# Kernel tuning notes

Measured on AMD Instinct MI355X. Metric: run time of the kernel, lower is better.

Reference implementation:

```python
import jax, jax.numpy as jnp
import numpy as np

N_NODES = 100000
N_EDGES = 1600000
EDGE_FEAT = 16
EDGE_HID = 32
NODE_FEAT = 128


def setup_inputs() -> dict:
    key = jax.random.key(0)
    ks = jax.random.split(key, 10)
    inp = {
        "edge_logits": jax.random.normal(ks[0], (N_EDGES, 1), dtype=jnp.float32),
        "edge_feats": jax.random.normal(ks[1], (N_EDGES, EDGE_FEAT), dtype=jnp.float32),
        "node_feats": jax.random.normal(ks[2], (N_NODES, NODE_FEAT), dtype=jnp.float32),
        "dst": jax.random.randint(ks[3], (N_EDGES,), 0, N_NODES, dtype=jnp.int32),
        # edge_transform Linear(edge_feat -> edge_hid)
        "W_et": jax.random.normal(ks[4], (EDGE_FEAT, EDGE_HID), dtype=jnp.float32) * (1.0 / np.sqrt(EDGE_FEAT)),
        "b_et": jnp.zeros((EDGE_HID,), dtype=jnp.float32),
        # MLP Linear(edge_hid + node_feat -> node_feat)
        "W1": jax.random.normal(ks[5], (EDGE_HID + NODE_FEAT, NODE_FEAT), dtype=jnp.float32) * (1.0 / np.sqrt(EDGE_HID + NODE_FEAT)),
        "b1": jnp.zeros((NODE_FEAT,), dtype=jnp.float32),
        # MLP Linear(node_feat -> node_feat)
        "W2": jax.random.normal(ks[6], (NODE_FEAT, NODE_FEAT), dtype=jnp.float32) * (1.0 / np.sqrt(NODE_FEAT)),
        "b2": jnp.zeros((NODE_FEAT,), dtype=jnp.float32),
    }
    return inp


def reference(edge_logits, edge_feats, node_feats, dst, W_et, b_et, W1, b1, W2, b2):
    # edge_softmax: segment softmax of edge_logits grouped by destination node
    logits = edge_logits[:, 0]                                        # [E]
    seg_max = jax.ops.segment_max(logits, dst, num_segments=N_NODES)  # [N]
    seg_max = jnp.where(jnp.isfinite(seg_max), seg_max, 0.0)          # guard empty segments
    ex = jnp.exp(logits - seg_max[dst])                               # [E]
    denom = jax.ops.segment_sum(ex, dst, num_segments=N_NODES)        # [N]
    denom = jnp.where(denom == 0.0, 1.0, denom)
    alpha = ex / denom[dst]                                           # [E]
    # edge transform (dropout is identity in eval) then weight by attention
    e = alpha[:, None] * (edge_feats @ W_et + b_et)                   # [E, H]
    # scatter-sum aggregation to destination nodes
    c = jax.ops.segment_sum(e, dst, num_segments=N_NODES)             # [N, H]
    context = jax.nn.elu(c)
    h = jnp.concatenate([context, node_feats], axis=1)                # [N, H+F]
    h = jax.nn.relu(h @ W1 + b1)
    return jax.nn.relu(h @ W2 + b2)                                   # [N, F]
```

## Files before the change

### kernel.cpp

```cpp
#include <hip/hip_runtime.h>

#define EF 16
#define EH 32
#define NF 128
#define K1 160
#define HS 168
#define H2S 136

typedef __attribute__((ext_vector_type(8))) short bf16x8;
typedef __attribute__((ext_vector_type(4))) float f32x4;

__device__ __forceinline__ unsigned short f2b(float f) {
  unsigned u = __float_as_uint(f);
  u += 0x7FFFu + ((u >> 16) & 1u);
  return (unsigned short)(u >> 16);
}
__device__ __forceinline__ unsigned pack2b(float a, float b) {
  return (unsigned)f2b(a) | ((unsigned)f2b(b) << 16);
}

__global__ void k_init(unsigned* __restrict__ cnt, int n,
                       const float* __restrict__ W1, const float* __restrict__ W2,
                       unsigned short* __restrict__ w1t, unsigned short* __restrict__ w2t) {
  int i = blockIdx.x * blockDim.x + threadIdx.x;
  if (i < n) cnt[i] = 0u;
  if (i < K1 * NF) {
    int nn = i / K1, k = i % K1;
    w1t[i] = f2b(W1[k * NF + nn]);
  } else if (i < K1 * NF + NF * NF) {
    int j = i - K1 * NF;
    int nn = j / NF, k = j % NF;
    w2t[j] = f2b(W2[k * NF + nn]);
  }
}

__global__ void k_hist(const int* __restrict__ dst, unsigned* __restrict__ cnt,
                       unsigned* __restrict__ rank, int n_edges) {
  int e = blockIdx.x * blockDim.x + threadIdx.x;
  if (e >= n_edges) return;
  rank[e] = atomicAdd(&cnt[dst[e]], 1u);
}

__global__ void k_scan1(const unsigned* __restrict__ cnt, unsigned* __restrict__ offs,
                        unsigned* __restrict__ bsum, int n) {
  __shared__ unsigned ts[256];
  int t = threadIdx.x;
  int base = blockIdx.x * 1024 + t * 4;
  unsigned v[4];
#pragma unroll
  for (int i = 0; i < 4; ++i) { int idx = base + i; v[i] = (idx < n) ? cnt[idx] : 0u; }
  unsigned run = 0;
#pragma unroll
  for (int i = 0; i < 4; ++i) { unsigned x = v[i]; v[i] = run; run += x; }
  ts[t] = run;
  __syncthreads();
  for (int off = 1; off < 256; off <<= 1) {
    unsigned add = (t >= off) ? ts[t - off] : 0u;
    __syncthreads();
    ts[t] += add;
    __syncthreads();
  }
  unsigned texcl = (t > 0) ? ts[t - 1] : 0u;
  if (t == 255) bsum[blockIdx.x] = ts[255];
#pragma unroll
  for (int i = 0; i < 4; ++i) { int idx = base + i; if (idx < n) offs[idx] = v[i] + texcl; }
}

__global__ void k_scan3(unsigned* __restrict__ offs, const unsigned* __restrict__ bsum,
                        int n, int nb) {
  __shared__ unsigned ts[256];
  int t = threadIdx.x;
  ts[t] = (t < nb) ? bsum[t] : 0u;
  __syncthreads();
  for (int off = 1; off < 256; off <<= 1) {
    unsigned add = (t >= off) ? ts[t - off] : 0u;
    __syncthreads();
    ts[t] += add;
    __syncthreads();
  }
  unsigned add = (blockIdx.x > 0) ? ts[blockIdx.x - 1] : 0u;
  int base = blockIdx.x * 1024 + t * 4;
#pragma unroll
  for (int i = 0; i < 4; ++i) { int idx = base + i; if (idx < n) offs[idx] += add; }
}

__global__ void k_scatter(const int* __restrict__ dst, const unsigned* __restrict__ rank,
                          const float* __restrict__ logits, const unsigned* __restrict__ offs,
                          const float* __restrict__ efeat,
                          unsigned* __restrict__ prodb, float* __restrict__ exs, int n_edges) {
  int e = blockIdx.x * blockDim.x + threadIdx.x;
  if (e >= n_edges) return;
  int d = dst[e];
  unsigned slot = offs[d] + rank[e];
  float ex = __expf(logits[e]);
  exs[slot] = ex;
  const float4* fp = (const float4*)(efeat + (size_t)e * EF);
  float4 v0 = fp[0], v1 = fp[1], v2 = fp[2], v3 = fp[3];
  uint4 o0, o1;
  o0.x = pack2b(ex * v0.x, ex * v0.y);
  o0.y = pack2b(ex * v0.z, ex * v0.w);
  o0.z = pack2b(ex * v1.x, ex * v1.y);
  o0.w = pack2b(ex * v1.z, ex * v1.w);
  o1.x = pack2b(ex * v2.x, ex * v2.y);
  o1.y = pack2b(ex * v2.z, ex * v2.w);
  o1.z = pack2b(ex * v3.x, ex * v3.y);
  o1.w = pack2b(ex * v3.z, ex * v3.w);
  uint4* pp = (uint4*)(prodb + (size_t)slot * 8);
  pp[0] = o0;
  pp[1] = o1;
}

__global__ __launch_bounds__(256) void k_gather(
    const unsigned* __restrict__ prodb, const float* __restrict__ exs,
    const unsigned* __restrict__ cnt, const unsigned* __restrict__ offs,
    const float* __restrict__ W_et, const float* __restrict__ b_et,
    unsigned short* __restrict__ ctxb, int n_nodes) {
  int node = (int)((blockIdx.x * blockDim.x + threadIdx.x) >> 6);
  if (node >= n_nodes) return;
  int lane = threadIdx.x & 63;
  unsigned start = offs[node];
  unsigned deg = cnt[node];
  int rg = lane >> 3, c = lane & 7;
  float a0 = 0.0f, a1 = 0.0f;
  for (unsigned i = rg; i < deg; i += 8) {
    unsigned p = prodb[(size_t)(start + i) * 8 + c];
    a0 += __uint_as_float(p << 16);
    a1 += __uint_as_float(p & 0xFFFF0000u);
  }
  a0 += __shfl_xor(a0, 8);  a1 += __shfl_xor(a1, 8);
  a0 += __shfl_xor(a0, 16); a1 += __shfl_xor(a1, 16);
  a0 += __shfl_xor(a0, 32); a1 += __shfl_xor(a1, 32);
  float dsum = 0.0f;
  for (unsigned i = lane; i < deg; i += 64) dsum += exs[start + i];
  dsum += __shfl_xor(dsum, 1);
  dsum += __shfl_xor(dsum, 2);
  dsum += __shfl_xor(dsum, 4);
  dsum += __shfl_xor(dsum, 8);
  dsum += __shfl_xor(dsum, 16);
  dsum += __shfl_xor(dsum, 32);
  float inv = (deg > 0) ? 1.0f / dsum : 0.0f;
  float S = (deg > 0) ? 1.0f : 0.0f;
  int j = lane & 31;
  float acc = 0.0f;
#pragma unroll
  for (int k = 0; k < 16; ++k) {
    float sk = (k & 1) ? __shfl(a1, k >> 1) : __shfl(a0, k >> 1);
    acc += sk * W_et[k * EH + j];
  }
  float cv = acc * inv + S * b_et[j];
  float ctxv = (cv > 0.0f) ? cv : (__expf(cv) - 1.0f);
  if (lane < 32) ctxb[(size_t)node * EH + lane] = f2b(ctxv);
}

__global__ __launch_bounds__(256) void k_node(
    const unsigned short* __restrict__ ctxb, const float* __restrict__ nf,
    const unsigned short* __restrict__ w1t, const unsigned short* __restrict__ w2t,
    const float* __restrict__ b1, const float* __restrict__ b2,
    float* __restrict__ out, int n_nodes) {
  __shared__ __align__(16) unsigned short hA[64 * HS];
  __shared__ __align__(16) unsigned short hB[64 * H2S];
  const int t = threadIdx.x;
  const int w = t >> 6, lane = t & 63;
  const int m = lane & 15, q = lane >> 4;
  int n0 = blockIdx.x * 64;
  if (n0 + 64 > n_nodes) n0 = n_nodes - 64;

  {
    int node = t >> 2, j = (t & 3) * 8;
    *(uint4*)&hA[node * HS + j] = *(const uint4*)&ctxb[(size_t)(n0 + node) * EH + j];
  }
#pragma unroll
  for (int i = 0; i < 8; ++i) {
    int idx = t + 256 * i;
    int node = idx >> 5, j = (idx & 31) * 4;
    float4 v = *(const float4*)&nf[(size_t)(n0 + node) * NF + j];
    unsigned short r[4] = {f2b(v.x), f2b(v.y), f2b(v.z), f2b(v.w)};
    *(uint2*)&hA[node * HS + EH + j] = *(const uint2*)r;
  }
  __syncthreads();

  const int mr = w * 16;
  f32x4 acc[8];
#pragma unroll
  for (int nt = 0; nt < 8; ++nt) acc[nt] = (f32x4){0.f, 0.f, 0.f, 0.f};
  for (int ks = 0; ks < 5; ++ks) {
    bf16x8 a = *(const bf16x8*)&hA[(mr + m) * HS + ks * 32 + q * 8];
#pragma unroll
    for (int nt = 0; nt < 8; ++nt) {
      bf16x8 b = *(const bf16x8*)&w1t[(size_t)(nt * 16 + m) * K1 + ks * 32 + q * 8];
      acc[nt] = __builtin_amdgcn_mfma_f32_16x16x32_bf16(a, b, acc[nt], 0, 0, 0);
    }
  }
#pragma unroll
  for (int nt = 0; nt < 8; ++nt) {
    float bb = b1[nt * 16 + m];
#pragma unroll
    for (int r = 0; r < 4; ++r) {
      float v = fmaxf(acc[nt][r] + bb, 0.0f);
      hB[(mr + q * 4 + r) * H2S + nt * 16 + m] = f2b(v);
    }
  }
  __syncthreads();

  f32x4 ac2[8];
#pragma unroll
  for (int nt = 0; nt < 8; ++nt) ac2[nt] = (f32x4){0.f, 0.f, 0.f, 0.f};
  for (int ks = 0; ks < 4; ++ks) {
    bf16x8 a = *(const bf16x8*)&hB[(mr + m) * H2S + ks * 32 + q * 8];
#pragma unroll
    for (int nt = 0; nt < 8; ++nt) {
      bf16x8 b = *(const bf16x8*)&w2t[(size_t)(nt * 16 + m) * NF + ks * 32 + q * 8];
      ac2[nt] = __builtin_amdgcn_mfma_f32_16x16x32_bf16(a, b, ac2[nt], 0, 0, 0);
    }
  }
#pragma unroll
  for (int nt = 0; nt < 8; ++nt) {
    float bb = b2[nt * 16 + m];
#pragma unroll
    for (int r = 0; r < 4; ++r) {
      out[(size_t)(n0 + mr + q * 4 + r) * NF + nt * 16 + m] = fmaxf(ac2[nt][r] + bb, 0.0f);
    }
  }
}

extern "C" void kernel_launch(void* const* d_in, const int* in_sizes, int n_in,
                              void* d_out, int out_size, void* d_ws, size_t ws_size,
                              hipStream_t stream) {
  const float* edge_logits = (const float*)d_in[0];
  const float* edge_feats  = (const float*)d_in[1];
  const float* node_feats  = (const float*)d_in[2];
  const int*   dst         = (const int*)d_in[3];
  const float* W_et        = (const float*)d_in[4];
  const float* b_et        = (const float*)d_in[5];
  const float* W1          = (const float*)d_in[6];
  const float* b1          = (const float*)d_in[7];
  const float* W2          = (const float*)d_in[8];
  const float* b2          = (const float*)d_in[9];
  float* out = (float*)d_out;

  const int E = in_sizes[0];
  const int n = in_sizes[2] / NF;

  unsigned* cnt   = (unsigned*)d_ws;
  unsigned* offs  = cnt + n;
  unsigned* bsum  = offs + n;
  unsigned* rank  = bsum + 256;
  float*    exs   = (float*)(rank + E);
  unsigned* prodb = (unsigned*)(exs + E);
  unsigned short* ctxb = (unsigned short*)(prodb + (size_t)E * 8);
  unsigned short* w1t  = ctxb + (size_t)n * EH;
  unsigned short* w2t  = w1t + NF * K1;

  const int thr = 256;
  const int nscan = (n + 1023) / 1024;

  k_init<<<(n + thr - 1) / thr, thr, 0, stream>>>(cnt, n, W1, W2, w1t, w2t);
  k_hist<<<(E + thr - 1) / thr, thr, 0, stream>>>(dst, cnt, rank, E);
  k_scan1<<<nscan, 256, 0, stream>>>(cnt, offs, bsum, n);
  k_scan3<<<nscan, 256, 0, stream>>>(offs, bsum, n, nscan);
  k_scatter<<<(E + thr - 1) / thr, thr, 0, stream>>>(dst, rank, edge_logits, offs, edge_feats,
                                                     prodb, exs, E);
  k_gather<<<(n * 64 + thr - 1) / thr, thr, 0, stream>>>(prodb, exs, cnt, offs,
                                                         W_et, b_et, ctxb, n);
  k_node<<<(n + 63) / 64, 256, 0, stream>>>(ctxb, node_feats, w1t, w2t, b1, b2, out, n);
}
```

Baseline: 428.9 us.

## Sort edges by index permutation and gather edge features in aggregation kernel

The scatter kernel no longer writes bf16 products of exp(logit) and edge features into destination-sorted order. It now writes only a compact (edge id, exp) pair per slot, and slots are assigned by an atomic cursor instead of a stored rank array. The gather kernel reads each edge's fp32 features indirectly through the permutation and computes the weighted sum and denominator in one pass. This removes the rank array, the exs array and the 32-byte-per-edge bf16 staging buffer, and it keeps fp32 precision. In exchange the gather now does random 64-byte reads of edge features, and the second atomic pass makes edge order within a segment nondeterministic.

```diff
diff --git a/kernel.cpp b/kernel.cpp
--- a/kernel.cpp
+++ b/kernel.cpp
@@ -14,9 +14,6 @@
   unsigned u = __float_as_uint(f);
   u += 0x7FFFu + ((u >> 16) & 1u);
   return (unsigned short)(u >> 16);
-}
-__device__ __forceinline__ unsigned pack2b(float a, float b) {
-  return (unsigned)f2b(a) | ((unsigned)f2b(b) << 16);
 }
 
 __global__ void k_init(unsigned* __restrict__ cnt, int n,
@@ -34,11 +31,10 @@
   }
 }
 
-__global__ void k_hist(const int* __restrict__ dst, unsigned* __restrict__ cnt,
-                       unsigned* __restrict__ rank, int n_edges) {
+__global__ void k_hist(const int* __restrict__ dst, unsigned* __restrict__ cnt, int n_edges) {
   int e = blockIdx.x * blockDim.x + threadIdx.x;
   if (e >= n_edges) return;
-  rank[e] = atomicAdd(&cnt[dst[e]], 1u);
+  atomicAdd(&cnt[dst[e]], 1u);
 }
 
 __global__ void k_scan1(const unsigned* __restrict__ cnt, unsigned* __restrict__ offs,
@@ -66,8 +62,8 @@
   for (int i = 0; i < 4; ++i) { int idx = base + i; if (idx < n) offs[idx] = v[i] + texcl; }
 }
 
-__global__ void k_scan3(unsigned* __restrict__ offs, const unsigned* __restrict__ bsum,
-                        int n, int nb) {
+__global__ void k_scan3(unsigned* __restrict__ offs, unsigned* __restrict__ cursor,
+                        const unsigned* __restrict__ bsum, int n, int nb) {
   __shared__ unsigned ts[256];
   int t = threadIdx.x;
   ts[t] = (t < nb) ? bsum[t] : 0u;
@@ -81,37 +77,24 @@
   unsigned add = (blockIdx.x > 0) ? ts[blockIdx.x - 1] : 0u;
   int base = blockIdx.x * 1024 + t * 4;
 #pragma unroll
-  for (int i = 0; i < 4; ++i) { int idx = base + i; if (idx < n) offs[idx] += add; }
-}
-
-__global__ void k_scatter(const int* __restrict__ dst, const unsigned* __restrict__ rank,
-                          const float* __restrict__ logits, const unsigned* __restrict__ offs,
-                          const float* __restrict__ efeat,
-                          unsigned* __restrict__ prodb, float* __restrict__ exs, int n_edges) {
+  for (int i = 0; i < 4; ++i) {
+    int idx = base + i;
+    if (idx < n) { unsigned v = offs[idx] + add; offs[idx] = v; cursor[idx] = v; }
+  }
+}
+
+__global__ void k_perm(const int* __restrict__ dst, const float* __restrict__ logits,
+                       unsigned* __restrict__ cursor, uint2* __restrict__ perm, int n_edges) {
   int e = blockIdx.x * blockDim.x + threadIdx.x;
   if (e >= n_edges) return;
   int d = dst[e];
-  unsigned slot = offs[d] + rank[e];
+  unsigned slot = atomicAdd(&cursor[d], 1u);
   float ex = __expf(logits[e]);
-  exs[slot] = ex;
-  const float4* fp = (const float4*)(efeat + (size_t)e * EF);
-  float4 v0 = fp[0], v1 = fp[1], v2 = fp[2], v3 = fp[3];
-  uint4 o0, o1;
-  o0.x = pack2b(ex * v0.x, ex * v0.y);
-  o0.y = pack2b(ex * v0.z, ex * v0.w);
-  o0.z = pack2b(ex * v1.x, ex * v1.y);
-  o0.w = pack2b(ex * v1.z, ex * v1.w);
-  o1.x = pack2b(ex * v2.x, ex * v2.y);
-  o1.y = pack2b(ex * v2.z, ex * v2.w);
-  o1.z = pack2b(ex * v3.x, ex * v3.y);
-  o1.w = pack2b(ex * v3.z, ex * v3.w);
-  uint4* pp = (uint4*)(prodb + (size_t)slot * 8);
-  pp[0] = o0;
-  pp[1] = o1;
+  perm[slot] = make_uint2((unsigned)e, __float_as_uint(ex));
 }
 
 __global__ __launch_bounds__(256) void k_gather(
-    const unsigned* __restrict__ prodb, const float* __restrict__ exs,
+    const uint2* __restrict__ perm, const float* __restrict__ efeat,
     const unsigned* __restrict__ cnt, const unsigned* __restrict__ offs,
     const float* __restrict__ W_et, const float* __restrict__ b_et,
     unsigned short* __restrict__ ctxb, int n_nodes) {
@@ -120,31 +103,24 @@
   int lane = threadIdx.x & 63;
   unsigned start = offs[node];
   unsigned deg = cnt[node];
-  int rg = lane >> 3, c = lane & 7;
-  float a0 = 0.0f, a1 = 0.0f;
-  for (unsigned i = rg; i < deg; i += 8) {
-    unsigned p = prodb[(size_t)(start + i) * 8 + c];
-    a0 += __uint_as_float(p << 16);
-    a1 += __uint_as_float(p & 0xFFFF0000u);
-  }
-  a0 += __shfl_xor(a0, 8);  a1 += __shfl_xor(a1, 8);
-  a0 += __shfl_xor(a0, 16); a1 += __shfl_xor(a1, 16);
-  a0 += __shfl_xor(a0, 32); a1 += __shfl_xor(a1, 32);
-  float dsum = 0.0f;
-  for (unsigned i = lane; i < deg; i += 64) dsum += exs[start + i];
-  dsum += __shfl_xor(dsum, 1);
-  dsum += __shfl_xor(dsum, 2);
-  dsum += __shfl_xor(dsum, 4);
-  dsum += __shfl_xor(dsum, 8);
-  dsum += __shfl_xor(dsum, 16);
-  dsum += __shfl_xor(dsum, 32);
+  int g = lane >> 4, c = lane & 15;
+  float a = 0.0f, dsum = 0.0f;
+  for (unsigned i = g; i < deg; i += 4) {
+    uint2 rec = perm[start + i];
+    float ex = __uint_as_float(rec.y);
+    float f = efeat[(size_t)rec.x * EF + c];
+    a += ex * f;
+    dsum += ex;
+  }
+  a += __shfl_xor(a, 16);      a += __shfl_xor(a, 32);
+  dsum += __shfl_xor(dsum, 16); dsum += __shfl_xor(dsum, 32);
   float inv = (deg > 0) ? 1.0f / dsum : 0.0f;
   float S = (deg > 0) ? 1.0f : 0.0f;
   int j = lane & 31;
   float acc = 0.0f;
 #pragma unroll
   for (int k = 0; k < 16; ++k) {
-    float sk = (k & 1) ? __shfl(a1, k >> 1) : __shfl(a0, k >> 1);
+    float sk = __shfl(a, k);
     acc += sk * W_et[k * EH + j];
   }
   float cv = acc * inv + S * b_et[j];
@@ -241,13 +217,12 @@
   const int E = in_sizes[0];
   const int n = in_sizes[2] / NF;
 
-  unsigned* cnt   = (unsigned*)d_ws;
-  unsigned* offs  = cnt + n;
-  unsigned* bsum  = offs + n;
-  unsigned* rank  = bsum + 256;
-  float*    exs   = (float*)(rank + E);
-  unsigned* prodb = (unsigned*)(exs + E);
-  unsigned short* ctxb = (unsigned short*)(prodb + (size_t)E * 8);
+  unsigned* cnt    = (unsigned*)d_ws;
+  unsigned* offs   = cnt + n;
+  unsigned* cursor = offs + n;
+  unsigned* bsum   = cursor + n;
+  uint2* perm = (uint2*)(((uintptr_t)(bsum + 256) + 7) & ~(uintptr_t)7);
+  unsigned short* ctxb = (unsigned short*)(perm + E);
   unsigned short* w1t  = ctxb + (size_t)n * EH;
   unsigned short* w2t  = w1t + NF * K1;
 
@@ -255,12 +230,11 @@
   const int nscan = (n + 1023) / 1024;
 
   k_init<<<(n + thr - 1) / thr, thr, 0, stream>>>(cnt, n, W1, W2, w1t, w2t);
-  k_hist<<<(E + thr - 1) / thr, thr, 0, stream>>>(dst, cnt, rank, E);
+  k_hist<<<(E + thr - 1) / thr, thr, 0, stream>>>(dst, cnt, E);
   k_scan1<<<nscan, 256, 0, stream>>>(cnt, offs, bsum, n);
-  k_scan3<<<nscan, 256, 0, stream>>>(offs, bsum, n, nscan);
-  k_scatter<<<(E + thr - 1) / thr, thr, 0, stream>>>(dst, rank, edge_logits, offs, edge_feats,
-                                                     prodb, exs, E);
-  k_gather<<<(n * 64 + thr - 1) / thr, thr, 0, stream>>>(prodb, exs, cnt, offs,
+  k_scan3<<<nscan, 256, 0, stream>>>(offs, cursor, bsum, n, nscan);
+  k_perm<<<(E + thr - 1) / thr, thr, 0, stream>>>(dst, edge_logits, cursor, perm, E);
+  k_gather<<<(n * 64 + thr - 1) / thr, thr, 0, stream>>>(perm, edge_feats, cnt, offs,
                                                          W_et, b_et, ctxb, n);
   k_node<<<(n + 63) / 64, 256, 0, stream>>>(ctxb, node_feats, w1t, w2t, b1, b2, out, n);
 }
```

Result: slower. 532.3 us (+24.1%).

## Partition scatter and gather by XCD so each die's L2 holds its node range

Applied to the files above, without the earlier changes.

The edge scatter becomes a kernel in which each block, assigned to one of eight XCDs by blockIdx&7, scans a chunk of edges and writes only those whose destination falls in that XCD's node range. The gather kernel maps nodes with the same XCD partition. The aim is that scattered writes and later reads of prodb stay in one die's L2 instead of spreading across all of them. In exchange, every edge's dst is read eight times, and the gather loop is unrolled by two with the prodb buffer aligned to 256 bytes.

```diff
diff --git a/kernel.cpp b/kernel.cpp
--- a/kernel.cpp
+++ b/kernel.cpp
@@ -84,45 +84,66 @@
   for (int i = 0; i < 4; ++i) { int idx = base + i; if (idx < n) offs[idx] += add; }
 }
 
-__global__ void k_scatter(const int* __restrict__ dst, const unsigned* __restrict__ rank,
-                          const float* __restrict__ logits, const unsigned* __restrict__ offs,
-                          const float* __restrict__ efeat,
-                          unsigned* __restrict__ prodb, float* __restrict__ exs, int n_edges) {
-  int e = blockIdx.x * blockDim.x + threadIdx.x;
-  if (e >= n_edges) return;
-  int d = dst[e];
-  unsigned slot = offs[d] + rank[e];
-  float ex = __expf(logits[e]);
-  exs[slot] = ex;
-  const float4* fp = (const float4*)(efeat + (size_t)e * EF);
-  float4 v0 = fp[0], v1 = fp[1], v2 = fp[2], v3 = fp[3];
-  uint4 o0, o1;
-  o0.x = pack2b(ex * v0.x, ex * v0.y);
-  o0.y = pack2b(ex * v0.z, ex * v0.w);
-  o0.z = pack2b(ex * v1.x, ex * v1.y);
-  o0.w = pack2b(ex * v1.z, ex * v1.w);
-  o1.x = pack2b(ex * v2.x, ex * v2.y);
-  o1.y = pack2b(ex * v2.z, ex * v2.w);
-  o1.z = pack2b(ex * v3.x, ex * v3.y);
-  o1.w = pack2b(ex * v3.z, ex * v3.w);
-  uint4* pp = (uint4*)(prodb + (size_t)slot * 8);
-  pp[0] = o0;
-  pp[1] = o1;
+__global__ __launch_bounds__(256) void k_prod(
+    const int* __restrict__ dst, const unsigned* __restrict__ rank,
+    const float* __restrict__ logits, const unsigned* __restrict__ offs,
+    const float* __restrict__ efeat,
+    unsigned* __restrict__ prodb, float* __restrict__ exs,
+    int n_edges, int nps, int n_nodes, int chunks) {
+  int xcd = blockIdx.x & 7;
+  int chunk = blockIdx.x >> 3;
+  int lo = xcd * nps;
+  int hi = min(lo + nps, n_nodes);
+  int per = (n_edges + chunks - 1) / chunks;
+  int e0 = chunk * per;
+  int e1 = min(e0 + per, n_edges);
+  for (int e = e0 + (int)threadIdx.x; e < e1; e += 256) {
+    int d = dst[e];
+    if (d >= lo && d < hi) {
+      unsigned slot = offs[d] + rank[e];
+      float ex = __expf(logits[e]);
+      exs[slot] = ex;
+      const float4* fp = (const float4*)(efeat + (size_t)e * EF);
+      float4 v0 = fp[0], v1 = fp[1], v2 = fp[2], v3 = fp[3];
+      uint4 o0, o1;
+      o0.x = pack2b(ex * v0.x, ex * v0.y);
+      o0.y = pack2b(ex * v0.z, ex * v0.w);
+      o0.z = pack2b(ex * v1.x, ex * v1.y);
+      o0.w = pack2b(ex * v1.z, ex * v1.w);
+      o1.x = pack2b(ex * v2.x, ex * v2.y);
+      o1.y = pack2b(ex * v2.z, ex * v2.w);
+      o1.z = pack2b(ex * v3.x, ex * v3.y);
+      o1.w = pack2b(ex * v3.z, ex * v3.w);
+      uint4* pp = (uint4*)(prodb + (size_t)slot * 8);
+      pp[0] = o0;
+      pp[1] = o1;
+    }
+  }
 }
 
 __global__ __launch_bounds__(256) void k_gather(
     const unsigned* __restrict__ prodb, const float* __restrict__ exs,
     const unsigned* __restrict__ cnt, const unsigned* __restrict__ offs,
     const float* __restrict__ W_et, const float* __restrict__ b_et,
-    unsigned short* __restrict__ ctxb, int n_nodes) {
-  int node = (int)((blockIdx.x * blockDim.x + threadIdx.x) >> 6);
-  if (node >= n_nodes) return;
+    unsigned short* __restrict__ ctxb, int nps, int n_nodes) {
+  int xcd = blockIdx.x & 7;
+  int idx = blockIdx.x >> 3;
+  int node = xcd * nps + (idx << 2) + (int)(threadIdx.x >> 6);
+  int node_end = min(xcd * nps + nps, n_nodes);
+  if (node >= node_end) return;
   int lane = threadIdx.x & 63;
   unsigned start = offs[node];
   unsigned deg = cnt[node];
   int rg = lane >> 3, c = lane & 7;
   float a0 = 0.0f, a1 = 0.0f;
-  for (unsigned i = rg; i < deg; i += 8) {
+  unsigned i = rg;
+  for (; i + 8 < deg; i += 16) {
+    unsigned p = prodb[(size_t)(start + i) * 8 + c];
+    unsigned q = prodb[(size_t)(start + i + 8) * 8 + c];
+    a0 += __uint_as_float(p << 16) + __uint_as_float(q << 16);
+    a1 += __uint_as_float(p & 0xFFFF0000u) + __uint_as_float(q & 0xFFFF0000u);
+  }
+  for (; i < deg; i += 8) {
     unsigned p = prodb[(size_t)(start + i) * 8 + c];
     a0 += __uint_as_float(p << 16);
     a1 += __uint_as_float(p & 0xFFFF0000u);
@@ -131,7 +152,7 @@
   a0 += __shfl_xor(a0, 16); a1 += __shfl_xor(a1, 16);
   a0 += __shfl_xor(a0, 32); a1 += __shfl_xor(a1, 32);
   float dsum = 0.0f;
-  for (unsigned i = lane; i < deg; i += 64) dsum += exs[start + i];
+  for (unsigned k = lane; k < deg; k += 64) dsum += exs[start + k];
   dsum += __shfl_xor(dsum, 1);
   dsum += __shfl_xor(dsum, 2);
   dsum += __shfl_xor(dsum, 4);
@@ -241,26 +262,28 @@
   const int E = in_sizes[0];
   const int n = in_sizes[2] / NF;
 
-  unsigned* cnt   = (unsigned*)d_ws;
-  unsigned* offs  = cnt + n;
-  unsigned* bsum  = offs + n;
-  unsigned* rank  = bsum + 256;
-  float*    exs   = (float*)(rank + E);
-  unsigned* prodb = (unsigned*)(exs + E);
+  unsigned* cnt  = (unsigned*)d_ws;
+  unsigned* offs = cnt + n;
+  unsigned* bsum = offs + n;
+  unsigned* rank = bsum + 256;
+  float*    exs  = (float*)(rank + E);
+  unsigned* prodb = (unsigned*)(((uintptr_t)(exs + E) + 255) & ~(uintptr_t)255);
   unsigned short* ctxb = (unsigned short*)(prodb + (size_t)E * 8);
   unsigned short* w1t  = ctxb + (size_t)n * EH;
   unsigned short* w2t  = w1t + NF * K1;
 
   const int thr = 256;
   const int nscan = (n + 1023) / 1024;
+  const int chunks = 256;
+  const int nps = (n + 7) >> 3;
 
   k_init<<<(n + thr - 1) / thr, thr, 0, stream>>>(cnt, n, W1, W2, w1t, w2t);
   k_hist<<<(E + thr - 1) / thr, thr, 0, stream>>>(dst, cnt, rank, E);
   k_scan1<<<nscan, 256, 0, stream>>>(cnt, offs, bsum, n);
   k_scan3<<<nscan, 256, 0, stream>>>(offs, bsum, n, nscan);
-  k_scatter<<<(E + thr - 1) / thr, thr, 0, stream>>>(dst, rank, edge_logits, offs, edge_feats,
-                                                     prodb, exs, E);
-  k_gather<<<(n * 64 + thr - 1) / thr, thr, 0, stream>>>(prodb, exs, cnt, offs,
-                                                         W_et, b_et, ctxb, n);
+  k_prod<<<chunks * 8, 256, 0, stream>>>(dst, rank, edge_logits, offs, edge_feats,
+                                         prodb, exs, E, nps, n, chunks);
+  const int gblocks = 8 * ((nps + 3) >> 2);
+  k_gather<<<gblocks, 256, 0, stream>>>(prodb, exs, cnt, offs, W_et, b_et, ctxb, nps, n);
   k_node<<<(n + 63) / 64, 256, 0, stream>>>(ctxb, node_feats, w1t, w2t, b1, b2, out, n);
 }
```

New measurement: 490.5 us. 14.4% more time.
